# Kernel optimization log

Measured on AMD Instinct MI355X. Metric: run time of the kernel, lower is better.

## Reference

```python
import jax, jax.numpy as jnp
import numpy as np

N = 50000
T = 6
E = 800000
F_IN = 64
HID = 64
HEADS = 4
NEG_SLOPE = 0.2
BN_EPS = 1e-5


def _gat_layer(x, src, dst, W, att_src, att_dst, bias, concat):
    # x: [N, Fin]; W: [Fin, H*C]; att_*: [H, C]; src/dst: [E+N] (self loops appended)
    n = x.shape[0]
    H, C = att_src.shape
    xl = (x @ W).reshape(n, H, C)                     # [N, H, C]
    a_src = jnp.sum(xl * att_src[None], axis=-1)      # [N, H]
    a_dst = jnp.sum(xl * att_dst[None], axis=-1)      # [N, H]
    e = jax.nn.leaky_relu(a_src[src] + a_dst[dst], NEG_SLOPE)  # [E', H]
    # segment softmax over destination nodes (every node has a self loop)
    m = jax.ops.segment_max(e, dst, num_segments=n)
    ex = jnp.exp(e - m[dst])
    s = jax.ops.segment_sum(ex, dst, num_segments=n)
    alpha = ex / (s[dst] + 1e-16)                     # [E', H]
    msg = alpha[:, :, None] * xl[src]                 # [E', H, C]
    out = jax.ops.segment_sum(msg, dst, num_segments=n)  # [N, H, C]
    if concat:
        out = out.reshape(n, H * C)
    else:
        out = out.mean(axis=1)
    return out + bias


def _forward(x_seq, edge_index, W1, as1, ad1, b1, W2, as2, ad2, b2,
             cw1, cb1, g1, be1, cw2, cb2, g2, be2, lw1, lb1, lw2, lb2):
    n = x_seq.shape[1]
    self_loop = jnp.arange(n, dtype=edge_index.dtype)
    src = jnp.concatenate([edge_index[0], self_loop])
    dst = jnp.concatenate([edge_index[1], self_loop])

    def per_t(x):
        h = _gat_layer(x, src, dst, W1, as1, ad1, b1, concat=True)
        h = jax.nn.elu(h)
        h = _gat_layer(h, src, dst, W2, as2, ad2, b2, concat=False)
        h = jax.nn.elu(h)
        return h                                      # [N, HID]

    temporal = jax.vmap(per_t)(x_seq)                 # [T, N, HID]
    temporal = jnp.transpose(temporal, (1, 2, 0))     # [N, HID, T]

    def conv_bn_relu(t, cw, cb, g, be):
        y = jax.lax.conv_general_dilated(
            t, cw, window_strides=(1,), padding=[(1, 1)],
            dimension_numbers=('NCH', 'OIH', 'NCH')) + cb[None, :, None]
        # BatchNorm1d in eval mode, running_mean=0, running_var=1
        y = y * (g / jnp.sqrt(1.0 + BN_EPS))[None, :, None] + be[None, :, None]
        return jax.nn.relu(y)

    t = conv_bn_relu(temporal, cw1, cb1, g1, be1)
    t = conv_bn_relu(t, cw2, cb2, g2, be2)
    pooled = t.mean(axis=-1)                          # adaptive avg pool -> [N, HID]
    h = jax.nn.relu(pooled @ lw1 + lb1)
    logits = h @ lw2 + lb2                            # [N, 1]
    return logits


def setup_inputs() -> dict:
    key = jax.random.key(0)
    ks = jax.random.split(key, 20)
    C1 = HID // HEADS  # 16
    s = 0.1
    return {
        'x_seq': jax.random.normal(ks[0], (T, N, F_IN), jnp.float32),
        'edge_index': jax.random.randint(ks[1], (2, E), 0, N, jnp.int32),
        'W1': jax.random.normal(ks[2], (F_IN, HEADS * C1), jnp.float32) * s,
        'as1': jax.random.normal(ks[3], (HEADS, C1), jnp.float32) * s,
        'ad1': jax.random.normal(ks[4], (HEADS, C1), jnp.float32) * s,
        'b1': jnp.zeros((HEADS * C1,), jnp.float32),
        'W2': jax.random.normal(ks[5], (HID, HEADS * HID), jnp.float32) * s,
        'as2': jax.random.normal(ks[6], (HEADS, HID), jnp.float32) * s,
        'ad2': jax.random.normal(ks[7], (HEADS, HID), jnp.float32) * s,
        'b2': jnp.zeros((HID,), jnp.float32),
        'cw1': jax.random.normal(ks[8], (HID, HID, 3), jnp.float32) * s,
        'cb1': jnp.zeros((HID,), jnp.float32),
        'g1': jnp.ones((HID,), jnp.float32),
        'be1': jnp.zeros((HID,), jnp.float32),
        'cw2': jax.random.normal(ks[9], (HID, HID, 3), jnp.float32) * s,
        'cb2': jnp.zeros((HID,), jnp.float32),
        'g2': jnp.ones((HID,), jnp.float32),
        'be2': jnp.zeros((HID,), jnp.float32),
        'lw1': jax.random.normal(ks[10], (HID, HID // 2), jnp.float32) * s,
        'lb1': jnp.zeros((HID // 2,), jnp.float32),
        'lw2': jax.random.normal(ks[11], (HID // 2, 1), jnp.float32) * s,
        'lb2': jnp.zeros((1,), jnp.float32),
    }


def reference(x_seq, edge_index, W1, as1, ad1, b1, W2, as2, ad2, b2,
              cw1, cb1, g1, be1, cw2, cb2, g2, be2, lw1, lb1, lw2, lb2):
    return _forward(x_seq, edge_index, W1, as1, ad1, b1, W2, as2, ad2, b2,
                    cw1, cb1, g1, be1, cw2, cb2, g2, be2, lw1, lb1, lw2, lb2)
```

## Files before the change

### kernel.cpp

```cpp
#include <hip/hip_runtime.h>
#include <math.h>

#define NN 50000
#define EE 800000
#define TT 6
#define SS (EE+NN)

__device__ __forceinline__ float lrelu(float x){ return x > 0.f ? x : 0.2f*x; }
__device__ __forceinline__ float eluf(float x){ return x > 0.f ? x : expm1f(x); }

__global__ void k_init_counts(int* __restrict__ c){
  int i = blockIdx.x*256 + threadIdx.x;
  if (i < NN) c[i] = 1;
}

__global__ void k_hist(const int* __restrict__ dst, int* __restrict__ c){
  int i = blockIdx.x*256 + threadIdx.x;
  if (i < EE) atomicAdd(&c[dst[i]], 1);
}

__global__ void k_scanA(const int* __restrict__ cnt, int* __restrict__ excl,
                        int* __restrict__ bsum){
  __shared__ int sh[1024];
  int tid = threadIdx.x;
  int i = blockIdx.x*1024 + tid;
  int v = (i < NN) ? cnt[i] : 0;
  int x = v;
  sh[tid] = x; __syncthreads();
  for (int off = 1; off < 1024; off <<= 1){
    int y = (tid >= off) ? sh[tid - off] : 0;
    __syncthreads();
    x += y; sh[tid] = x; __syncthreads();
  }
  if (i < NN) excl[i] = x - v;
  if (tid == 1023) bsum[blockIdx.x] = x;
}

__global__ void k_scanB(int* __restrict__ bsum, int nb){
  if (threadIdx.x == 0){
    int run = 0;
    for (int b = 0; b < nb; ++b){ int t = bsum[b]; bsum[b] = run; run += t; }
  }
}

__global__ void k_scanC(const int* __restrict__ excl, const int* __restrict__ bsum,
                        int* __restrict__ rowptr, int* __restrict__ cursor){
  int i = blockIdx.x*1024 + threadIdx.x;
  if (i < NN){
    int v = excl[i] + bsum[blockIdx.x];
    rowptr[i] = v; cursor[i] = v;
  }
  if (i == 0) rowptr[NN] = SS;
}

__global__ void k_scatter(const int* __restrict__ ei, int* __restrict__ cursor,
                          int* __restrict__ csr, int* __restrict__ dstOf){
  int i = blockIdx.x*256 + threadIdx.x;
  if (i < EE){
    int d = ei[EE + i];
    int p = atomicAdd(&cursor[d], 1);
    csr[p] = ei[i];
    dstOf[p] = d;
  } else if (i < SS){
    int v = i - EE;
    int p = atomicAdd(&cursor[v], 1);
    csr[p] = v;
    dstOf[p] = v;
  }
}

__global__ void k_prep(const float* __restrict__ W1, const float* __restrict__ as1,
                       const float* __restrict__ ad1,
                       const float* __restrict__ W2, const float* __restrict__ as2,
                       const float* __restrict__ ad2,
                       const float* __restrict__ cw1, const float* __restrict__ cw2,
                       const float* __restrict__ lw1,
                       float* __restrict__ Was1, float* __restrict__ Wad1,
                       float* __restrict__ Wat2, float* __restrict__ Wb,
                       float4* __restrict__ wq1, float4* __restrict__ wq2,
                       float* __restrict__ lw1t){
  int tid = threadIdx.x;
  int k = tid >> 2, h = tid & 3;
  float s1 = 0.f, d1 = 0.f, s2 = 0.f, d2 = 0.f;
  for (int c = 0; c < 16; ++c){
    float w = W1[k*64 + h*16 + c];
    s1 += w * as1[h*16 + c];
    d1 += w * ad1[h*16 + c];
  }
  for (int c = 0; c < 64; ++c){
    float w = W2[k*256 + h*64 + c];
    s2 += w * as2[h*64 + c];
    d2 += w * ad2[h*64 + c];
  }
  Was1[k*4+h] = s1; Wad1[k*4+h] = d1;
  Wat2[k*8 + h] = s2; Wat2[k*8 + 4 + h] = d2;
  for (int idx = tid; idx < 256*64; idx += 256){
    int kf = idx >> 6, c = idx & 63;
    int hh = kf >> 6, kk = kf & 63;
    Wb[idx] = W2[kk*256 + hh*64 + c];
  }
  for (int idx = tid; idx < 64*64; idx += 256){
    int i = idx >> 6, o = idx & 63;
    wq1[idx] = make_float4(cw1[o*192+i*3], cw1[o*192+i*3+1], cw1[o*192+i*3+2], 0.f);
    wq2[idx] = make_float4(cw2[o*192+i*3], cw2[o*192+i*3+1], cw2[o*192+i*3+2], 0.f);
  }
  for (int idx = tid; idx < 32*64; idx += 256){
    int j = idx >> 6, kk = idx & 63;
    lw1t[idx] = lw1[kk*32 + j];
  }
}

__global__ __launch_bounds__(256) void k_gemm_att1(const float* __restrict__ A,
                            const float* __restrict__ W,
                            const float* __restrict__ Was, const float* __restrict__ Wad,
                            float* __restrict__ Xl, float* __restrict__ a_src,
                            float* __restrict__ a_dst){
  __shared__ float At[64][16];
  int tid = threadIdx.x;
  int r0 = blockIdx.x * 16;
  {
    const float4* A4 = (const float4*)(A + (size_t)r0*64);
    float4 v = A4[tid];
    int r = tid >> 4, k4 = (tid & 15) << 2;
    At[k4+0][r] = v.x; At[k4+1][r] = v.y;
    At[k4+2][r] = v.z; At[k4+3][r] = v.w;
  }
  __syncthreads();
  int col = tid & 63;
  int rbase = (tid >> 6) << 2;
  float acc0=0.f, acc1=0.f, acc2=0.f, acc3=0.f;
  for (int k = 0; k < 64; ++k){
    float w = W[k*64 + col];
    float4 a4 = *(const float4*)&At[k][rbase];
    acc0 += a4.x*w; acc1 += a4.y*w; acc2 += a4.z*w; acc3 += a4.w*w;
  }
  Xl[(size_t)(r0+rbase+0)*64 + col] = acc0;
  Xl[(size_t)(r0+rbase+1)*64 + col] = acc1;
  Xl[(size_t)(r0+rbase+2)*64 + col] = acc2;
  Xl[(size_t)(r0+rbase+3)*64 + col] = acc3;
  if (tid < 128){
    int r = tid >> 3, jx = tid & 7;
    int h = jx & 3;
    const float* Wv = (jx < 4) ? Was : Wad;
    float a = 0.f;
    for (int k = 0; k < 64; ++k) a += At[k][r] * Wv[k*4 + h];
    if (jx < 4) a_src[(r0 + r)*4 + h] = a;
    else        a_dst[(r0 + r)*4 + h] = a;
  }
}

__global__ __launch_bounds__(256) void k_edge1(const int* __restrict__ csr,
                        const int* __restrict__ dstOf,
                        const float* __restrict__ a_src, const float* __restrict__ a_dst,
                        float* __restrict__ peh){
  int k = blockIdx.x*256 + threadIdx.x;
  if (k >= SS) return;
  int sn = csr[k], dn = dstOf[k];
  float4 as = ((const float4*)a_src)[sn];
  float4 ad = ((const float4*)a_dst)[dn];
  peh[k]                 = __expf(lrelu(as.x+ad.x));
  peh[(size_t)SS + k]    = __expf(lrelu(as.y+ad.y));
  peh[2*(size_t)SS + k]  = __expf(lrelu(as.z+ad.z));
  peh[3*(size_t)SS + k]  = __expf(lrelu(as.w+ad.w));
}

__global__ __launch_bounds__(256) void k_edge2(const int* __restrict__ csr,
                        const int* __restrict__ dstOf,
                        const float* __restrict__ a_src, const float* __restrict__ a_dst,
                        float4* __restrict__ pe4){
  int k = blockIdx.x*256 + threadIdx.x;
  if (k >= SS) return;
  int sn = csr[k], dn = dstOf[k];
  float4 as = ((const float4*)a_src)[sn];
  float4 ad = ((const float4*)a_dst)[dn];
  pe4[k] = make_float4(__expf(lrelu(as.x+ad.x)), __expf(lrelu(as.y+ad.y)),
                       __expf(lrelu(as.z+ad.z)), __expf(lrelu(as.w+ad.w)));
}

__global__ __launch_bounds__(256) void k_agg1(
                       const float* __restrict__ xl, const float* __restrict__ peh,
                       const float* __restrict__ b1, const float* __restrict__ Wat2,
                       const int* __restrict__ rowptr, const int* __restrict__ csr,
                       float* __restrict__ h1,
                       float* __restrict__ a_src2, float* __restrict__ a_dst2){
  int lane = threadIdx.x & 63;
  int wid  = __builtin_amdgcn_readfirstlane(threadIdx.x >> 6);
  int n = blockIdx.x*4 + wid;
  int h = lane >> 4;
  const float* __restrict__ ph = peh + (size_t)h*SS;
  int rs = rowptr[n], re = rowptr[n+1];
  float s = 0.f, acc = 0.f;
  int j = rs;
  for (; j + 4 <= re; j += 4){
    int sn0=csr[j], sn1=csr[j+1], sn2=csr[j+2], sn3=csr[j+3];
    float p0=ph[j], p1=ph[j+1], p2=ph[j+2], p3=ph[j+3];
    float x0=xl[(size_t)sn0*64+lane], x1=xl[(size_t)sn1*64+lane];
    float x2=xl[(size_t)sn2*64+lane], x3=xl[(size_t)sn3*64+lane];
    s += p0; acc += p0*x0;
    s += p1; acc += p1*x1;
    s += p2; acc += p2*x2;
    s += p3; acc += p3*x3;
  }
  for (; j < re; ++j){
    int sn = csr[j];
    float p = ph[j];
    float x = xl[(size_t)sn*64 + lane];
    s += p; acc += p*x;
  }
  float hv = eluf(acc/(s + 1e-16f) + b1[lane]);
  h1[(size_t)n*64 + lane] = hv;
  float4 wA = ((const float4*)Wat2)[lane*2];
  float4 wB = ((const float4*)Wat2)[lane*2 + 1];
  float p[8];
  p[0]=hv*wA.x; p[1]=hv*wA.y; p[2]=hv*wA.z; p[3]=hv*wA.w;
  p[4]=hv*wB.x; p[5]=hv*wB.y; p[6]=hv*wB.z; p[7]=hv*wB.w;
#pragma unroll
  for (int off = 32; off >= 1; off >>= 1){
#pragma unroll
    for (int q = 0; q < 8; ++q) p[q] += __shfl_xor(p[q], off);
  }
  if (lane == 0){
    ((float4*)a_src2)[n] = make_float4(p[0],p[1],p[2],p[3]);
    ((float4*)a_dst2)[n] = make_float4(p[4],p[5],p[6],p[7]);
  }
}

__global__ __launch_bounds__(256) void k_agg2(
                       const float* __restrict__ h1, const float4* __restrict__ pe4,
                       const int* __restrict__ rowptr, const int* __restrict__ csr,
                       float* __restrict__ agg){
  int lane = threadIdx.x & 63;
  int wid  = __builtin_amdgcn_readfirstlane(threadIdx.x >> 6);
  int n = blockIdx.x*4 + wid;
  int rs = rowptr[n], re = rowptr[n+1];
  float s0=0.f,s1=0.f,s2=0.f,s3=0.f;
  float g0=0.f,g1=0.f,g2=0.f,g3=0.f;
  int j = rs;
  for (; j + 4 <= re; j += 4){
    int sa=csr[j], sb=csr[j+1], sc=csr[j+2], sd=csr[j+3];
    float4 pa = pe4[j];
    float4 pb = pe4[j+1];
    float4 pc = pe4[j+2];
    float4 pd = pe4[j+3];
    float xa = h1[(size_t)sa*64 + lane];
    float xb = h1[(size_t)sb*64 + lane];
    float xc = h1[(size_t)sc*64 + lane];
    float xd = h1[(size_t)sd*64 + lane];
    s0 += pa.x+pb.x+pc.x+pd.x; g0 += pa.x*xa + pb.x*xb + pc.x*xc + pd.x*xd;
    s1 += pa.y+pb.y+pc.y+pd.y; g1 += pa.y*xa + pb.y*xb + pc.y*xc + pd.y*xd;
    s2 += pa.z+pb.z+pc.z+pd.z; g2 += pa.z*xa + pb.z*xb + pc.z*xc + pd.z*xd;
    s3 += pa.w+pb.w+pc.w+pd.w; g3 += pa.w*xa + pb.w*xb + pc.w*xc + pd.w*xd;
  }
  for (; j < re; ++j){
    int sn = csr[j];
    float4 pv = pe4[j];
    float x = h1[(size_t)sn*64 + lane];
    s0 += pv.x; g0 += pv.x*x;
    s1 += pv.y; g1 += pv.y*x;
    s2 += pv.z; g2 += pv.z*x;
    s3 += pv.w; g3 += pv.w*x;
  }
  size_t base = (size_t)n*256 + lane;
  agg[base      ] = g0/(s0 + 1e-16f);
  agg[base +  64] = g1/(s1 + 1e-16f);
  agg[base + 128] = g2/(s2 + 1e-16f);
  agg[base + 192] = g3/(s3 + 1e-16f);
}

__global__ __launch_bounds__(256) void k_out2(const float* __restrict__ agg,
                                              const float* __restrict__ Wb,
                                              const float* __restrict__ b2,
                                              float* __restrict__ ht){
  __shared__ float A[64*257];
  int tid = threadIdx.x;
  int lane = tid & 63;
  int w = __builtin_amdgcn_readfirstlane(tid >> 6);
  int r0 = blockIdx.x * 64;
  for (int jj = 0; jj < 64; ++jj){
    int m = jj*256 + tid;
    int row = m >> 8, k = m & 255;
    int rsrc = r0 + row; if (rsrc >= NN) rsrc = NN-1;
    A[row*257 + k] = agg[(size_t)rsrc*256 + k];
  }
  __syncthreads();
  const float* __restrict__ Wbw = Wb + w*16;
  float acc[16];
#pragma unroll
  for (int jq = 0; jq < 16; ++jq) acc[jq] = 0.f;
  const float* Ar = A + lane*257;
#pragma unroll 8
  for (int k = 0; k < 256; ++k){
    float a = Ar[k];
#pragma unroll
    for (int jq = 0; jq < 16; ++jq) acc[jq] += a * Wbw[(k<<6) + jq];
  }
  __syncthreads();
#pragma unroll
  for (int jq = 0; jq < 16; ++jq){
    int c = w*16 + jq;
    A[lane*65 + c] = eluf(0.25f*acc[jq] + b2[c]);
  }
  __syncthreads();
  for (int jj = 0; jj < 16; ++jj){
    int m = jj*256 + tid;
    int row = m >> 6, c = m & 63;
    int rdst = r0 + row;
    if (rdst < NN) ht[(size_t)rdst*64 + c] = A[row*65 + c];
  }
}

__global__ __launch_bounds__(256) void k_conv(const float* __restrict__ htb,
    const float4* __restrict__ wq1, const float* __restrict__ cb1,
    const float* __restrict__ g1,   const float* __restrict__ be1,
    const float4* __restrict__ wq2, const float* __restrict__ cb2,
    const float* __restrict__ g2,   const float* __restrict__ be2,
    float* __restrict__ pooledG){
  __shared__ float X[64*199];
  int tid  = threadIdx.x;
  int lane = tid & 63;
  int w    = __builtin_amdgcn_readfirstlane(tid >> 6);
  int nn   = lane & 31;
  int ch2  = lane >> 5;
  int n0 = blockIdx.x*32;
  int n  = n0 + nn;
  int ob = w*16 + ch2*8;

#pragma unroll
  for (int it = 0; it < 8; ++it){
    int ns = it*4 + w;
    int nsrc = n0 + ns; if (nsrc >= NN) nsrc = NN-1;
    float xv[6];
#pragma unroll
    for (int t = 0; t < 6; ++t) xv[t] = htb[((size_t)t*NN + nsrc)*64 + lane];
#pragma unroll
    for (int t = 0; t < 6; ++t) X[lane*199 + t*33 + ns] = xv[t];
  }
  __syncthreads();

  float acc[8][6];
#pragma unroll
  for (int q = 0; q < 8; ++q){
    float c = cb1[ob+q];
#pragma unroll
    for (int t = 0; t < 6; ++t) acc[q][t] = c;
  }
  for (int i = 0; i < 64; ++i){
    const float* xp = X + i*199 + nn;
    float x1 = xp[0], x2 = xp[33], x3 = xp[66];
    float x4 = xp[99], x5 = xp[132], x6 = xp[165];
    const float4* wrow = wq1 + (i<<6) + ob;
#pragma unroll
    for (int q = 0; q < 8; ++q){
      float4 wv = wrow[q];
      acc[q][0] += wv.y*x1 + wv.z*x2;
      acc[q][1] += wv.x*x1 + wv.y*x2 + wv.z*x3;
      acc[q][2] += wv.x*x2 + wv.y*x3 + wv.z*x4;
      acc[q][3] += wv.x*x3 + wv.y*x4 + wv.z*x5;
      acc[q][4] += wv.x*x4 + wv.y*x5 + wv.z*x6;
      acc[q][5] += wv.x*x5 + wv.y*x6;
    }
  }
  __syncthreads();
#pragma unroll
  for (int q = 0; q < 8; ++q){
    float bns = g1[ob+q]*rsqrtf(1.f + 1e-5f), be = be1[ob+q];
    float* xp = X + (ob+q)*199 + nn;
#pragma unroll
    for (int t = 0; t < 6; ++t) xp[t*33] = fmaxf(acc[q][t]*bns + be, 0.f);
  }
  __syncthreads();

#pragma unroll
  for (int q = 0; q < 8; ++q){
    float c = cb2[ob+q];
#pragma unroll
    for (int t = 0; t < 6; ++t) acc[q][t] = c;
  }
  for (int i = 0; i < 64; ++i){
    const float* xp = X + i*199 + nn;
    float x1 = xp[0], x2 = xp[33], x3 = xp[66];
    float x4 = xp[99], x5 = xp[132], x6 = xp[165];
    const float4* wrow = wq2 + (i<<6) + ob;
#pragma unroll
    for (int q = 0; q < 8; ++q){
      float4 wv = wrow[q];
      acc[q][0] += wv.y*x1 + wv.z*x2;
      acc[q][1] += wv.x*x1 + wv.y*x2 + wv.z*x3;
      acc[q][2] += wv.x*x2 + wv.y*x3 + wv.z*x4;
      acc[q][3] += wv.x*x3 + wv.y*x4 + wv.z*x5;
      acc[q][4] += wv.x*x4 + wv.y*x5 + wv.z*x6;
      acc[q][5] += wv.x*x5 + wv.y*x6;
    }
  }
  if (n < NN){
#pragma unroll
    for (int q = 0; q < 8; ++q){
      float bns = g2[ob+q]*rsqrtf(1.f + 1e-5f), be = be2[ob+q];
      float pooled = 0.f;
#pragma unroll
      for (int t = 0; t < 6; ++t) pooled += fmaxf(acc[q][t]*bns + be, 0.f);
      pooledG[(size_t)(ob+q)*NN + n] = pooled*(1.f/6.f);
    }
  }
}

__global__ __launch_bounds__(256) void k_mlp(const float* __restrict__ pooledG,
    const float* __restrict__ lw1t, const float* __restrict__ lb1,
    const float* __restrict__ lw2,  const float* __restrict__ lb2,
    float* __restrict__ out){
  int lane = threadIdx.x & 63;
  int w = __builtin_amdgcn_readfirstlane(threadIdx.x >> 6);
  int n = (blockIdx.x*4 + w)*64 + lane;
  int nc = (n < NN) ? n : (NN-1);
  float p[64];
#pragma unroll 16
  for (int o = 0; o < 64; ++o) p[o] = pooledG[(size_t)o*NN + nc];
  float po = 0.f;
  for (int j = 0; j < 32; ++j){
    float hj = lb1[j];
#pragma unroll 16
    for (int k = 0; k < 64; ++k) hj += p[k] * lw1t[j*64 + k];
    po += fmaxf(hj, 0.f) * lw2[j];
  }
  if (n < NN) out[n] = po + lb2[0];
}

extern "C" void kernel_launch(void* const* d_in, const int* in_sizes, int n_in,
                              void* d_out, int out_size, void* d_ws, size_t ws_size,
                              hipStream_t stream) {
  const float* x_seq = (const float*)d_in[0];
  const int*   ei    = (const int*)  d_in[1];
  const float* W1  = (const float*)d_in[2];
  const float* as1 = (const float*)d_in[3];
  const float* ad1 = (const float*)d_in[4];
  const float* b1  = (const float*)d_in[5];
  const float* W2  = (const float*)d_in[6];
  const float* as2 = (const float*)d_in[7];
  const float* ad2 = (const float*)d_in[8];
  const float* b2  = (const float*)d_in[9];
  const float* cw1 = (const float*)d_in[10];
  const float* cb1 = (const float*)d_in[11];
  const float* g1  = (const float*)d_in[12];
  const float* be1 = (const float*)d_in[13];
  const float* cw2 = (const float*)d_in[14];
  const float* cb2 = (const float*)d_in[15];
  const float* g2  = (const float*)d_in[16];
  const float* be2 = (const float*)d_in[17];
  const float* lw1 = (const float*)d_in[18];
  const float* lb1 = (const float*)d_in[19];
  const float* lw2 = (const float*)d_in[20];
  const float* lb2 = (const float*)d_in[21];
  float* out = (float*)d_out;

  char* wp = (char*)d_ws;
  auto alloc = [&](size_t bytes) -> char* {
    char* p = wp; wp += (bytes + 255) & ~(size_t)255; return p;
  };
  int*   counts = (int*)  alloc(NN*sizeof(int));
  int*   excl   = (int*)  alloc(NN*sizeof(int));
  int*   bsum   = (int*)  alloc(64*sizeof(int));
  int*   rowptr = (int*)  alloc((NN+1)*sizeof(int));
  int*   cursor = (int*)  alloc(NN*sizeof(int));
  int*   csr    = (int*)  alloc((size_t)SS*sizeof(int));
  int*   dstOf  = (int*)  alloc((size_t)SS*sizeof(int));
  float* peh    = (float*)alloc((size_t)4*SS*sizeof(float));
  float4* pe4   = (float4*)alloc((size_t)SS*sizeof(float4));
  float* a_src1 = (float*)alloc((size_t)NN*4*sizeof(float));
  float* a_dst1 = (float*)alloc((size_t)NN*4*sizeof(float));
  float* a_src2 = (float*)alloc((size_t)NN*4*sizeof(float));
  float* a_dst2 = (float*)alloc((size_t)NN*4*sizeof(float));
  float* h1     = (float*)alloc((size_t)NN*64*sizeof(float));
  float* agg    = (float*)alloc((size_t)NN*256*sizeof(float));
  float* xl1    = agg;
  float* htb    = (float*)alloc((size_t)TT*NN*64*sizeof(float));
  float* pooledG= (float*)alloc((size_t)64*NN*sizeof(float));
  float* Was1 = (float*)alloc(256*sizeof(float));
  float* Wad1 = (float*)alloc(256*sizeof(float));
  float* Wat2 = (float*)alloc(64*8*sizeof(float));
  float* Wb   = (float*)alloc(256*64*sizeof(float));
  float4* wq1 = (float4*)alloc(64*64*sizeof(float4));
  float4* wq2 = (float4*)alloc(64*64*sizeof(float4));
  float* lw1t = (float*)alloc(32*64*sizeof(float));

  const int NBSCAN = (NN + 1023)/1024;
  k_init_counts<<<(NN+255)/256, 256, 0, stream>>>(counts);
  k_hist<<<(EE+255)/256, 256, 0, stream>>>(ei + EE, counts);
  k_scanA<<<NBSCAN, 1024, 0, stream>>>(counts, excl, bsum);
  k_scanB<<<1, 64, 0, stream>>>(bsum, NBSCAN);
  k_scanC<<<NBSCAN, 1024, 0, stream>>>(excl, bsum, rowptr, cursor);
  k_scatter<<<(SS+255)/256, 256, 0, stream>>>(ei, cursor, csr, dstOf);
  k_prep<<<1, 256, 0, stream>>>(W1, as1, ad1, W2, as2, ad2, cw1, cw2, lw1,
                                Was1, Wad1, Wat2, Wb, wq1, wq2, lw1t);

  const int NEDGE = (SS + 255)/256;
  const int NOUT2 = (NN + 63)/64;
  for (int t = 0; t < TT; ++t){
    const float* xt = x_seq + (size_t)t*NN*64;
    k_gemm_att1<<<NN/16, 256, 0, stream>>>(xt, W1, Was1, Wad1, xl1, a_src1, a_dst1);
    k_edge1<<<NEDGE, 256, 0, stream>>>(csr, dstOf, a_src1, a_dst1, peh);
    k_agg1<<<NN/4, 256, 0, stream>>>(xl1, peh, b1, Wat2, rowptr, csr,
                                     h1, a_src2, a_dst2);
    k_edge2<<<NEDGE, 256, 0, stream>>>(csr, dstOf, a_src2, a_dst2, pe4);
    k_agg2<<<NN/4, 256, 0, stream>>>(h1, pe4, rowptr, csr, agg);
    k_out2<<<NOUT2, 256, 0, stream>>>(agg, Wb, b2, htb + (size_t)t*NN*64);
  }
  k_conv<<<(NN+31)/32, 256, 0, stream>>>(htb, wq1, cb1, g1, be1, wq2, cb2, g2, be2,
                                         pooledG);
  k_mlp<<<(NN+255)/256, 256, 0, stream>>>(pooledG, lw1t, lb1, lw2, lb2, out);
}
```

Baseline: 1.408 ms.

## Unroll gather loops by 8, vectorize LDS reads in out2, retile temporal conv

The edge-gather loops in both GAT aggregation kernels are unrolled from 4 to 8 edges per iteration, so more independent neighbour loads are in flight at once. The out2 GEMM pads its LDS rows to 260 floats and reads four activations per float4 load. The temporal conv kernel now handles 16 nodes per block with 4 output channels per thread, using a smaller LDS tile and float2-grouped accumulators, which cuts registers per thread and launches more blocks. The risks are higher register pressure in the gather loops and extra weight loads per output in the conv kernel.

```diff
diff --git a/kernel.cpp b/kernel.cpp
--- a/kernel.cpp
+++ b/kernel.cpp
@@ -191,15 +191,23 @@
   int rs = rowptr[n], re = rowptr[n+1];
   float s = 0.f, acc = 0.f;
   int j = rs;
-  for (; j + 4 <= re; j += 4){
-    int sn0=csr[j], sn1=csr[j+1], sn2=csr[j+2], sn3=csr[j+3];
-    float p0=ph[j], p1=ph[j+1], p2=ph[j+2], p3=ph[j+3];
+  for (; j + 8 <= re; j += 8){
+    int sn0=csr[j],   sn1=csr[j+1], sn2=csr[j+2], sn3=csr[j+3];
+    int sn4=csr[j+4], sn5=csr[j+5], sn6=csr[j+6], sn7=csr[j+7];
+    float p0=ph[j],   p1=ph[j+1], p2=ph[j+2], p3=ph[j+3];
+    float p4=ph[j+4], p5=ph[j+5], p6=ph[j+6], p7=ph[j+7];
     float x0=xl[(size_t)sn0*64+lane], x1=xl[(size_t)sn1*64+lane];
     float x2=xl[(size_t)sn2*64+lane], x3=xl[(size_t)sn3*64+lane];
+    float x4=xl[(size_t)sn4*64+lane], x5=xl[(size_t)sn5*64+lane];
+    float x6=xl[(size_t)sn6*64+lane], x7=xl[(size_t)sn7*64+lane];
     s += p0; acc += p0*x0;
     s += p1; acc += p1*x1;
     s += p2; acc += p2*x2;
     s += p3; acc += p3*x3;
+    s += p4; acc += p4*x4;
+    s += p5; acc += p5*x5;
+    s += p6; acc += p6*x6;
+    s += p7; acc += p7*x7;
   }
   for (; j < re; ++j){
     int sn = csr[j];
@@ -236,20 +244,33 @@
   float s0=0.f,s1=0.f,s2=0.f,s3=0.f;
   float g0=0.f,g1=0.f,g2=0.f,g3=0.f;
   int j = rs;
-  for (; j + 4 <= re; j += 4){
-    int sa=csr[j], sb=csr[j+1], sc=csr[j+2], sd=csr[j+3];
+  for (; j + 8 <= re; j += 8){
+    int sa=csr[j],   sb=csr[j+1], sc=csr[j+2], sd=csr[j+3];
+    int se=csr[j+4], sf=csr[j+5], sg=csr[j+6], sh2=csr[j+7];
     float4 pa = pe4[j];
     float4 pb = pe4[j+1];
     float4 pc = pe4[j+2];
     float4 pd = pe4[j+3];
+    float4 pe = pe4[j+4];
+    float4 pf = pe4[j+5];
+    float4 pg = pe4[j+6];
+    float4 pq = pe4[j+7];
     float xa = h1[(size_t)sa*64 + lane];
     float xb = h1[(size_t)sb*64 + lane];
     float xc = h1[(size_t)sc*64 + lane];
     float xd = h1[(size_t)sd*64 + lane];
-    s0 += pa.x+pb.x+pc.x+pd.x; g0 += pa.x*xa + pb.x*xb + pc.x*xc + pd.x*xd;
-    s1 += pa.y+pb.y+pc.y+pd.y; g1 += pa.y*xa + pb.y*xb + pc.y*xc + pd.y*xd;
-    s2 += pa.z+pb.z+pc.z+pd.z; g2 += pa.z*xa + pb.z*xb + pc.z*xc + pd.z*xd;
-    s3 += pa.w+pb.w+pc.w+pd.w; g3 += pa.w*xa + pb.w*xb + pc.w*xc + pd.w*xd;
+    float xe = h1[(size_t)se*64 + lane];
+    float xf = h1[(size_t)sf*64 + lane];
+    float xg = h1[(size_t)sg*64 + lane];
+    float xh = h1[(size_t)sh2*64 + lane];
+    s0 += pa.x+pb.x+pc.x+pd.x+pe.x+pf.x+pg.x+pq.x;
+    g0 += pa.x*xa + pb.x*xb + pc.x*xc + pd.x*xd + pe.x*xe + pf.x*xf + pg.x*xg + pq.x*xh;
+    s1 += pa.y+pb.y+pc.y+pd.y+pe.y+pf.y+pg.y+pq.y;
+    g1 += pa.y*xa + pb.y*xb + pc.y*xc + pd.y*xd + pe.y*xe + pf.y*xf + pg.y*xg + pq.y*xh;
+    s2 += pa.z+pb.z+pc.z+pd.z+pe.z+pf.z+pg.z+pq.z;
+    g2 += pa.z*xa + pb.z*xb + pc.z*xc + pd.z*xd + pe.z*xe + pf.z*xf + pg.z*xg + pq.z*xh;
+    s3 += pa.w+pb.w+pc.w+pd.w+pe.w+pf.w+pg.w+pq.w;
+    g3 += pa.w*xa + pb.w*xb + pc.w*xc + pd.w*xd + pe.w*xe + pf.w*xf + pg.w*xg + pq.w*xh;
   }
   for (; j < re; ++j){
     int sn = csr[j];
@@ -271,7 +292,7 @@
                                               const float* __restrict__ Wb,
                                               const float* __restrict__ b2,
                                               float* __restrict__ ht){
-  __shared__ float A[64*257];
+  __shared__ float A[64*260];
   int tid = threadIdx.x;
   int lane = tid & 63;
   int w = __builtin_amdgcn_readfirstlane(tid >> 6);
@@ -280,19 +301,21 @@
     int m = jj*256 + tid;
     int row = m >> 8, k = m & 255;
     int rsrc = r0 + row; if (rsrc >= NN) rsrc = NN-1;
-    A[row*257 + k] = agg[(size_t)rsrc*256 + k];
+    A[row*260 + k] = agg[(size_t)rsrc*256 + k];
   }
   __syncthreads();
   const float* __restrict__ Wbw = Wb + w*16;
   float acc[16];
 #pragma unroll
   for (int jq = 0; jq < 16; ++jq) acc[jq] = 0.f;
-  const float* Ar = A + lane*257;
-#pragma unroll 8
-  for (int k = 0; k < 256; ++k){
-    float a = Ar[k];
-#pragma unroll
-    for (int jq = 0; jq < 16; ++jq) acc[jq] += a * Wbw[(k<<6) + jq];
+  const float* Ar = A + lane*260;
+  for (int k = 0; k < 256; k += 4){
+    float4 a4 = *(const float4*)&Ar[k];
+#pragma unroll
+    for (int jq = 0; jq < 16; ++jq){
+      acc[jq] += a4.x*Wbw[(k  )*64 + jq] + a4.y*Wbw[(k+1)*64 + jq]
+               + a4.z*Wbw[(k+2)*64 + jq] + a4.w*Wbw[(k+3)*64 + jq];
+    }
   }
   __syncthreads();
 #pragma unroll
@@ -315,90 +338,100 @@
     const float4* __restrict__ wq2, const float* __restrict__ cb2,
     const float* __restrict__ g2,   const float* __restrict__ be2,
     float* __restrict__ pooledG){
-  __shared__ float X[64*199];
+  __shared__ float X[64*103];
   int tid  = threadIdx.x;
   int lane = tid & 63;
   int w    = __builtin_amdgcn_readfirstlane(tid >> 6);
-  int nn   = lane & 31;
-  int ch2  = lane >> 5;
-  int n0 = blockIdx.x*32;
+  int nn   = lane & 15;
+  int oq   = lane >> 4;
+  int n0 = blockIdx.x*16;
   int n  = n0 + nn;
-  int ob = w*16 + ch2*8;
-
-#pragma unroll
-  for (int it = 0; it < 8; ++it){
-    int ns = it*4 + w;
-    int nsrc = n0 + ns; if (nsrc >= NN) nsrc = NN-1;
+  int ob = w*16 + oq*4;
+
+#pragma unroll
+  for (int k = 0; k < 4; ++k){
+    int p  = k*256 + tid;
+    int ch = p & 63, ns = p >> 6;
     float xv[6];
 #pragma unroll
-    for (int t = 0; t < 6; ++t) xv[t] = htb[((size_t)t*NN + nsrc)*64 + lane];
-#pragma unroll
-    for (int t = 0; t < 6; ++t) X[lane*199 + t*33 + ns] = xv[t];
-  }
-  __syncthreads();
-
-  float acc[8][6];
-#pragma unroll
-  for (int q = 0; q < 8; ++q){
+    for (int t = 0; t < 6; ++t) xv[t] = htb[((size_t)t*NN + n0 + ns)*64 + ch];
+#pragma unroll
+    for (int t = 0; t < 6; ++t) X[ch*103 + t*17 + ns] = xv[t];
+  }
+  __syncthreads();
+
+  float2 a12[4], a34[4];
+  float a0[4], a5[4];
+#pragma unroll
+  for (int q = 0; q < 4; ++q){
     float c = cb1[ob+q];
-#pragma unroll
-    for (int t = 0; t < 6; ++t) acc[q][t] = c;
+    a0[q]=c; a5[q]=c; a12[q]=make_float2(c,c); a34[q]=make_float2(c,c);
   }
   for (int i = 0; i < 64; ++i){
-    const float* xp = X + i*199 + nn;
-    float x1 = xp[0], x2 = xp[33], x3 = xp[66];
-    float x4 = xp[99], x5 = xp[132], x6 = xp[165];
-    const float4* wrow = wq1 + (i<<6) + ob;
-#pragma unroll
-    for (int q = 0; q < 8; ++q){
-      float4 wv = wrow[q];
-      acc[q][0] += wv.y*x1 + wv.z*x2;
-      acc[q][1] += wv.x*x1 + wv.y*x2 + wv.z*x3;
-      acc[q][2] += wv.x*x2 + wv.y*x3 + wv.z*x4;
-      acc[q][3] += wv.x*x3 + wv.y*x4 + wv.z*x5;
-      acc[q][4] += wv.x*x4 + wv.y*x5 + wv.z*x6;
-      acc[q][5] += wv.x*x5 + wv.y*x6;
+    const float* xp = X + i*103 + nn;
+    float x1 = xp[0], x2 = xp[17], x3 = xp[34];
+    float x4 = xp[51], x5 = xp[68], x6 = xp[85];
+    float2 x12 = make_float2(x1,x2), x23 = make_float2(x2,x3);
+    float2 x34 = make_float2(x3,x4), x45 = make_float2(x4,x5);
+    float2 x56 = make_float2(x5,x6);
+#pragma unroll
+    for (int q = 0; q < 4; ++q){
+      float4 wv = wq1[(i<<6) + ob + q];
+      a0[q] += wv.y*x1 + wv.z*x2;
+      a12[q].x += wv.x*x12.x + wv.y*x23.x + wv.z*x34.x;
+      a12[q].y += wv.x*x12.y + wv.y*x23.y + wv.z*x34.y;
+      a34[q].x += wv.x*x34.x + wv.y*x45.x + wv.z*x56.x;
+      a34[q].y += wv.x*x34.y + wv.y*x45.y + wv.z*x56.y;
+      a5[q] += wv.x*x5 + wv.y*x6;
     }
   }
   __syncthreads();
 #pragma unroll
-  for (int q = 0; q < 8; ++q){
+  for (int q = 0; q < 4; ++q){
     float bns = g1[ob+q]*rsqrtf(1.f + 1e-5f), be = be1[ob+q];
-    float* xp = X + (ob+q)*199 + nn;
-#pragma unroll
-    for (int t = 0; t < 6; ++t) xp[t*33] = fmaxf(acc[q][t]*bns + be, 0.f);
-  }
-  __syncthreads();
-
-#pragma unroll
-  for (int q = 0; q < 8; ++q){
+    float* xp = X + (ob+q)*103 + nn;
+    xp[0]   = fmaxf(a0[q]   *bns + be, 0.f);
+    xp[17]  = fmaxf(a12[q].x*bns + be, 0.f);
+    xp[34]  = fmaxf(a12[q].y*bns + be, 0.f);
+    xp[51]  = fmaxf(a34[q].x*bns + be, 0.f);
+    xp[68]  = fmaxf(a34[q].y*bns + be, 0.f);
+    xp[85]  = fmaxf(a5[q]   *bns + be, 0.f);
+  }
+  __syncthreads();
+
+#pragma unroll
+  for (int q = 0; q < 4; ++q){
     float c = cb2[ob+q];
-#pragma unroll
-    for (int t = 0; t < 6; ++t) acc[q][t] = c;
+    a0[q]=c; a5[q]=c; a12[q]=make_float2(c,c); a34[q]=make_float2(c,c);
   }
   for (int i = 0; i < 64; ++i){
-    const float* xp = X + i*199 + nn;
-    float x1 = xp[0], x2 = xp[33], x3 = xp[66];
-    float x4 = xp[99], x5 = xp[132], x6 = xp[165];
-    const float4* wrow = wq2 + (i<<6) + ob;
-#pragma unroll
-    for (int q = 0; q < 8; ++q){
-      float4 wv = wrow[q];
-      acc[q][0] += wv.y*x1 + wv.z*x2;
-      acc[q][1] += wv.x*x1 + wv.y*x2 + wv.z*x3;
-      acc[q][2] += wv.x*x2 + wv.y*x3 + wv.z*x4;
-      acc[q][3] += wv.x*x3 + wv.y*x4 + wv.z*x5;
-      acc[q][4] += wv.x*x4 + wv.y*x5 + wv.z*x6;
-      acc[q][5] += wv.x*x5 + wv.y*x6;
+    const float* xp = X + i*103 + nn;
+    float x1 = xp[0], x2 = xp[17], x3 = xp[34];
+    float x4 = xp[51], x5 = xp[68], x6 = xp[85];
+    float2 x12 = make_float2(x1,x2), x23 = make_float2(x2,x3);
+    float2 x34 = make_float2(x3,x4), x45 = make_float2(x4,x5);
+    float2 x56 = make_float2(x5,x6);
+#pragma unroll
+    for (int q = 0; q < 4; ++q){
+      float4 wv = wq2[(i<<6) + ob + q];
+      a0[q] += wv.y*x1 + wv.z*x2;
+      a12[q].x += wv.x*x12.x + wv.y*x23.x + wv.z*x34.x;
+      a12[q].y += wv.x*x12.y + wv.y*x23.y + wv.z*x34.y;
+      a34[q].x += wv.x*x34.x + wv.y*x45.x + wv.z*x56.x;
+      a34[q].y += wv.x*x34.y + wv.y*x45.y + wv.z*x56.y;
+      a5[q] += wv.x*x5 + wv.y*x6;
     }
   }
   if (n < NN){
 #pragma unroll
-    for (int q = 0; q < 8; ++q){
+    for (int q = 0; q < 4; ++q){
       float bns = g2[ob+q]*rsqrtf(1.f + 1e-5f), be = be2[ob+q];
-      float pooled = 0.f;
-#pragma unroll
-      for (int t = 0; t < 6; ++t) pooled += fmaxf(acc[q][t]*bns + be, 0.f);
+      float pooled = fmaxf(a0[q]   *bns + be, 0.f)
+                   + fmaxf(a12[q].x*bns + be, 0.f)
+                   + fmaxf(a12[q].y*bns + be, 0.f)
+                   + fmaxf(a34[q].x*bns + be, 0.f)
+                   + fmaxf(a34[q].y*bns + be, 0.f)
+                   + fmaxf(a5[q]   *bns + be, 0.f);
       pooledG[(size_t)(ob+q)*NN + n] = pooled*(1.f/6.f);
     }
   }
@@ -504,7 +537,7 @@
     k_agg2<<<NN/4, 256, 0, stream>>>(h1, pe4, rowptr, csr, agg);
     k_out2<<<NOUT2, 256, 0, stream>>>(agg, Wb, b2, htb + (size_t)t*NN*64);
   }
-  k_conv<<<(NN+31)/32, 256, 0, stream>>>(htb, wq1, cb1, g1, be1, wq2, cb2, g2, be2,
-                                         pooledG);
+  k_conv<<<NN/16, 256, 0, stream>>>(htb, wq1, cb1, g1, be1, wq2, cb2, g2, be2,
+                                    pooledG);
   k_mlp<<<(NN+255)/256, 256, 0, stream>>>(pooledG, lw1t, lb1, lw2, lb2, out);
 }
```

Result: slower. 1.442 ms (+2.4%).
